# Performance work log

Hardware: AMD Instinct MI355X
Metric: run time of the kernel (lower is better)

Reference implementation:

```python
import jax, jax.numpy as jnp
import numpy as np

D_MODEL = 256
SCALE = jnp.sqrt(jnp.float32(D_MODEL))


def setup_inputs() -> dict:
    key = jax.random.key(0)
    kq, kk, kv = jax.random.split(key, 3)
    B, S, D = 4, 4096, D_MODEL
    Q = jax.random.normal(kq, (B, S, D), dtype=jnp.float32)
    K = jax.random.normal(kk, (B, S, D), dtype=jnp.float32)
    V = jax.random.normal(kv, (B, S, D), dtype=jnp.float32)
    return {"Q": Q, "K": K, "V": V}


def reference(Q, K, V):
    # scores: (B, S, S) = Q @ K^T / sqrt(d_model)
    scores = jnp.einsum('bqd,bkd->bqk', Q, K) / SCALE
    attn = jax.nn.softmax(scores, axis=-1)
    # output: (B, S, D)
    return jnp.einsum('bqk,bkd->bqd', attn, V)
```

## Files before the change

### kernel.cpp

```cpp
#include <hip/hip_runtime.h>
#include <hip/hip_bf16.h>
#include <stdint.h>

#define S_LEN 4096
#define D_DIM 256
#define NBATCH 4
#define NSUP 32

typedef unsigned short u16;
typedef float  f32x4  __attribute__((ext_vector_type(4)));
typedef __bf16 bf16x8 __attribute__((ext_vector_type(8)));
typedef __bf16 bf16x4 __attribute__((ext_vector_type(4)));
typedef short  s16x8  __attribute__((ext_vector_type(8)));
typedef short  s16x4  __attribute__((ext_vector_type(4)));

#define AS1 __attribute__((address_space(1)))
#define AS3 __attribute__((address_space(3)))

__device__ __forceinline__ f32x4 mfma16(bf16x8 a, bf16x8 b, f32x4 c) {
  return __builtin_amdgcn_mfma_f32_16x16x32_bf16(a, b, c, 0, 0, 0);
}

__device__ __forceinline__ s16x4 cvt4(float x, float y, float z, float w) {
  bf16x4 b;
  b[0] = (__bf16)x; b[1] = (__bf16)y; b[2] = (__bf16)z; b[3] = (__bf16)w;
  return __builtin_bit_cast(s16x4, b);
}

__device__ __forceinline__ void gload16(const void* g, void* l) {
  __builtin_amdgcn_global_load_lds((const AS1 unsigned int*)g,
                                   (AS3 unsigned int*)l, 16, 0, 0);
}


__global__ void build_kimg(const float* __restrict__ K, u16* __restrict__ img) {
  const int wg  = blockIdx.x;
  const int tid = threadIdx.x;
  const float* src = K + (size_t)wg * 64 * D_DIM;
  u16*         dst = img + (size_t)wg * 16384;
  #pragma unroll
  for (int i = 0; i < 8; ++i) {
    const int idx = i * 256 + tid;
    const int k = idx >> 5, p = idx & 31;
    const int q = p ^ (k & 7);
    const float* s = src + k * 256 + q * 8;
    float4 f0 = *reinterpret_cast<const float4*>(s);
    float4 f1 = *reinterpret_cast<const float4*>(s + 4);
    s16x8 v = __builtin_shufflevector(cvt4(f0.x, f0.y, f0.z, f0.w),
                                      cvt4(f1.x, f1.y, f1.z, f1.w),
                                      0, 1, 2, 3, 4, 5, 6, 7);
    *reinterpret_cast<s16x8*>(dst + k * 256 + p * 8) = v;
  }
}

__global__ void build_vimg(const float* __restrict__ V, u16* __restrict__ img) {
  __shared__ u16 lds[64 * 264];
  const int wg  = blockIdx.x;
  const int tid = threadIdx.x;
  const float* src = V + (size_t)wg * 64 * D_DIM;
  u16*         dst = img + (size_t)wg * 16384;
  #pragma unroll
  for (int i = 0; i < 8; ++i) {
    const int idx = i * 256 + tid;
    const int k = idx >> 5, q = idx & 31;
    const float* s = src + k * 256 + q * 8;
    float4 f0 = *reinterpret_cast<const float4*>(s);
    float4 f1 = *reinterpret_cast<const float4*>(s + 4);
    s16x8 v = __builtin_shufflevector(cvt4(f0.x, f0.y, f0.z, f0.w),
                                      cvt4(f1.x, f1.y, f1.z, f1.w),
                                      0, 1, 2, 3, 4, 5, 6, 7);
    *reinterpret_cast<s16x8*>(&lds[k * 264 + q * 8]) = v;
  }
  __syncthreads();
  #pragma unroll
  for (int i = 0; i < 8; ++i) {
    const int idx = i * 256 + tid;
    const int d = idx >> 3, c = idx & 7;
    const int cp = c ^ (d & 7);
    s16x8 o;
    #pragma unroll
    for (int j = 0; j < 8; ++j) {
      const int col = 8 * cp + j;
      const int k = (col & 3) + 4 * (col >> 4) + 16 * ((col >> 2) & 3);
      o[j] = (short)lds[k * 264 + d];
    }
    *reinterpret_cast<s16x8*>(dst + d * 64 + c * 8) = o;
  }
}

__device__ __forceinline__
void compute_tile(const char* KsB, const char* vpA, const char* vpB,
                  const bf16x8 (&qf)[8], f32x4 (&acc)[16],
                  float& m_run, float& l_run, int g, int h)
{
  const f32x4 fz = {0.f, 0.f, 0.f, 0.f};

  f32x4 st[4];
  __builtin_amdgcn_s_setprio(1);
  #pragma unroll
  for (int t = 0; t < 4; ++t) {
    f32x4 a = fz;
    const int row = t * 16 + h;
    const int sw  = (row & 7) << 4;
    #pragma unroll
    for (int dc = 0; dc < 8; ++dc) {
      s16x8 kfrag = *reinterpret_cast<const s16x8*>(KsB + row * 512 + ((dc * 64 + g * 16) ^ sw));
      a = mfma16(__builtin_bit_cast(bf16x8, kfrag), qf[dc], a);
    }
    st[t] = a;
  }
  __builtin_amdgcn_s_setprio(0);

  float sv[16];
  #pragma unroll
  for (int t = 0; t < 4; ++t) {
    sv[t * 4 + 0] = st[t][0]; sv[t * 4 + 1] = st[t][1];
    sv[t * 4 + 2] = st[t][2]; sv[t * 4 + 3] = st[t][3];
  }
  float tmax = sv[0];
  #pragma unroll
  for (int i = 1; i < 16; ++i) tmax = fmaxf(tmax, sv[i]);
  tmax = fmaxf(tmax, __shfl_xor(tmax, 16));
  tmax = fmaxf(tmax, __shfl_xor(tmax, 32));

  if (!__all(tmax <= m_run + 8.0f)) {
    const float mnew  = fmaxf(m_run, tmax);
    const float alpha = __expf(m_run - mnew);
    l_run *= alpha;
    const float af0 = __shfl(alpha, g * 4 + 0);
    const float af1 = __shfl(alpha, g * 4 + 1);
    const float af2 = __shfl(alpha, g * 4 + 2);
    const float af3 = __shfl(alpha, g * 4 + 3);
    #pragma unroll
    for (int dt = 0; dt < 16; ++dt) {
      acc[dt][0] *= af0; acc[dt][1] *= af1; acc[dt][2] *= af2; acc[dt][3] *= af3;
    }
    m_run = mnew;
  }

  float psum = 0.f;
  #pragma unroll
  for (int i = 0; i < 16; ++i) { sv[i] = __expf(sv[i] - m_run); psum += sv[i]; }
  psum += __shfl_xor(psum, 16);
  psum += __shfl_xor(psum, 32);
  l_run += psum;

  bf16x8 pa0, pa1;
  #pragma unroll
  for (int j = 0; j < 8; ++j) { pa0[j] = (__bf16)sv[j]; pa1[j] = (__bf16)sv[8 + j]; }

  __builtin_amdgcn_s_setprio(1);
  #pragma unroll
  for (int dt = 0; dt < 16; ++dt) {
    s16x8 v0 = *reinterpret_cast<const s16x8*>(vpA + dt * 2048);
    s16x8 v1 = *reinterpret_cast<const s16x8*>(vpB + dt * 2048);
    acc[dt] = mfma16(pa0, __builtin_bit_cast(bf16x8, v0), acc[dt]);
    acc[dt] = mfma16(pa1, __builtin_bit_cast(bf16x8, v1), acc[dt]);
  }
  __builtin_amdgcn_s_setprio(0);
}

__device__ __forceinline__
void stage_img(const u16* KimgB, const u16* VimgB, int T,
               char* KsB, char* VtB, int w, int lane)
{
  const char* ks = (const char*)(KimgB + (size_t)T * 16384) + lane * 16;
  const char* vs = (const char*)(VimgB + (size_t)T * 16384) + lane * 16;
  #pragma unroll
  for (int i = 0; i < 8; ++i) {
    const int off = (i * 4 + w) * 1024;
    gload16(ks + off, KsB + off);
    gload16(vs + off, VtB + off);
  }
}

template<bool USE_WS>
__global__ __launch_bounds__(512, 1)
void attn_fwd_kernel(const float* __restrict__ Qg, const void* __restrict__ Kp,
                     const void* __restrict__ Vp, float* __restrict__ Og)
{
  __shared__ __align__(16) char smem[131072];

  const int wg   = blockIdx.x;
  const int swz  = (wg & 7) * 32 + (wg >> 3);
  const int b    = swz >> 6;
  const int qt   = swz & 63;
  const int tid  = threadIdx.x;
  const int wave = tid >> 6;
  const int lane = tid & 63;
  const int g    = lane >> 4;
  const int h    = lane & 15;
  const int gid  = tid >> 8;
  const int ltid = tid & 255;
  const int wq   = wave & 3;
  const int w    = wave & 3;

  const int kb  = ltid & 15;
  const int dcq = ltid >> 4;
  const int Xw  = 32 * (kb & 3) + 8 * (kb >> 2);

  char* KsB = smem + gid * 65536;
  char* VtB = KsB + 32768;

  const int qbase = qt * 64 + wq * 16;

  bf16x8 qf[8];
  {
    const float* qrow = Qg + ((size_t)b * S_LEN + qbase + h) * D_DIM;
    #pragma unroll
    for (int dc = 0; dc < 8; ++dc) {
      float4 f0 = *reinterpret_cast<const float4*>(qrow + dc * 32 + g * 8);
      float4 f1 = *reinterpret_cast<const float4*>(qrow + dc * 32 + g * 8 + 4);
      bf16x8 q;
      q[0] = (__bf16)(f0.x * 0.0625f); q[1] = (__bf16)(f0.y * 0.0625f);
      q[2] = (__bf16)(f0.z * 0.0625f); q[3] = (__bf16)(f0.w * 0.0625f);
      q[4] = (__bf16)(f1.x * 0.0625f); q[5] = (__bf16)(f1.y * 0.0625f);
      q[6] = (__bf16)(f1.z * 0.0625f); q[7] = (__bf16)(f1.w * 0.0625f);
      qf[dc] = q;
    }
  }

  f32x4 acc[16];
  const f32x4 fz = {0.f, 0.f, 0.f, 0.f};
  #pragma unroll
  for (int i = 0; i < 16; ++i) acc[i] = fz;
  float m_run = -1e30f;
  float l_run = 0.f;

  const char* vpA = VtB + h * 128 + ((32 * g)      ^ ((h & 7) << 4));
  const char* vpB = VtB + h * 128 + ((32 * g + 16) ^ ((h & 7) << 4));

  if constexpr (USE_WS) {
    const u16* KimgB = (const u16*)Kp + (size_t)b * 64 * 16384;
    const u16* VimgB = (const u16*)Vp + (size_t)b * 64 * 16384;

    if (gid == 0) stage_img(KimgB, VimgB, 0, KsB, VtB, w, lane);
    __syncthreads();

    for (int s = 0; s < NSUP; ++s) {
      if (gid == 0) compute_tile(KsB, vpA, vpB, qf, acc, m_run, l_run, g, h);
      else          stage_img(KimgB, VimgB, 2 * s + 1, KsB, VtB, w, lane);
      __syncthreads();
      if (gid == 0) { if (s < NSUP - 1) stage_img(KimgB, VimgB, 2 * s + 2, KsB, VtB, w, lane); }
      else          compute_tile(KsB, vpA, vpB, qf, acc, m_run, l_run, g, h);
      __syncthreads();
    }

  } else {
    const float* Kf = (const float*)Kp + (size_t)b * S_LEN * D_DIM;
    const float* Vf = (const float*)Vp + (size_t)b * S_LEN * D_DIM;
    for (int s = 0; s < NSUP; ++s) {
      const int kt = 2 * s + gid;
      __syncthreads();
      #pragma unroll
      for (int i = 0; i < 16; ++i) {
        int flat = i * 256 + ltid;
        int kk = flat >> 6;
        int d  = (flat & 63) * 4;
        float4 fk = *reinterpret_cast<const float4*>(Kf + (size_t)(kt * 64 + kk) * D_DIM + d);
        *reinterpret_cast<s16x4*>(KsB + kk * 512 + ((d * 2) ^ ((kk & 7) << 4))) = cvt4(fk.x, fk.y, fk.z, fk.w);
      }
      {
        s16x8 lo[4], hi[4];
        #pragma unroll
        for (int r = 0; r < 4; ++r) {
          const float* src = Vf + (size_t)(kt * 64 + kb * 4 + r) * D_DIM + dcq * 16;
          float4 f0 = *reinterpret_cast<const float4*>(src);
          float4 f1 = *reinterpret_cast<const float4*>(src + 4);
          float4 f2 = *reinterpret_cast<const float4*>(src + 8);
          float4 f3 = *reinterpret_cast<const float4*>(src + 12);
          lo[r] = __builtin_shufflevector(cvt4(f0.x, f0.y, f0.z, f0.w),
                                          cvt4(f1.x, f1.y, f1.z, f1.w), 0, 1, 2, 3, 4, 5, 6, 7);
          hi[r] = __builtin_shufflevector(cvt4(f2.x, f2.y, f2.z, f2.w),
                                          cvt4(f3.x, f3.y, f3.z, f3.w), 0, 1, 2, 3, 4, 5, 6, 7);
        }
        #pragma unroll
        for (int j = 0; j < 8; ++j) {
          s16x4 c0, c1;
          c0[0] = lo[0][j]; c0[1] = lo[1][j]; c0[2] = lo[2][j]; c0[3] = lo[3][j];
          c1[0] = hi[0][j]; c1[1] = hi[1][j]; c1[2] = hi[2][j]; c1[3] = hi[3][j];
          const int d0 = dcq * 16 + j;
          const int d1 = d0 + 8;
          *reinterpret_cast<s16x4*>(VtB + d0 * 128 + (Xw ^ ((d0 & 7) << 4))) = c0;
          *reinterpret_cast<s16x4*>(VtB + d1 * 128 + (Xw ^ ((d1 & 7) << 4))) = c1;
        }
      }
      __syncthreads();
      compute_tile(KsB, vpA, vpB, qf, acc, m_run, l_run, g, h);
    }
  }

  __syncthreads();
  float2* mlM = reinterpret_cast<float2*>(smem + 65536);
  if (gid == 1) {
    const int bw = wave - 4;
    char* base = smem + bw * 16384 + lane * 256;
    #pragma unroll
    for (int dt = 0; dt < 16; ++dt) {
      float4 v; v.x = acc[dt][0]; v.y = acc[dt][1]; v.z = acc[dt][2]; v.w = acc[dt][3];
      *reinterpret_cast<float4*>(base + (dt * 16 ^ ((lane & 7) << 4))) = v;
    }
    if (g == 0) { float2 ml; ml.x = m_run; ml.y = l_run; mlM[bw * 16 + h] = ml; }
  }
  __syncthreads();
  if (gid == 0) {
    const float2 ml = mlM[wave * 16 + h];
    const float mB = ml.x, lB = ml.y;
    const float m  = fmaxf(m_run, mB);
    const float sA = __expf(m_run - m);
    const float sB = __expf(mB - m);
    const float l  = l_run * sA + lB * sB;
    float aA[4], aB[4], inv[4];
    #pragma unroll
    for (int r = 0; r < 4; ++r) {
      aA[r]  = __shfl(sA, g * 4 + r);
      aB[r]  = __shfl(sB, g * 4 + r);
      inv[r] = 1.f / __shfl(l, g * 4 + r);
    }
    const char* base = smem + wave * 16384 + lane * 256;
    float* orow0 = Og + ((size_t)b * S_LEN + qbase) * D_DIM;
    #pragma unroll
    for (int dt = 0; dt < 16; ++dt) {
      float4 ab = *reinterpret_cast<const float4*>(base + (dt * 16 ^ ((lane & 7) << 4)));
      orow0[(size_t)(g * 4 + 0) * D_DIM + h + dt * 16] = (acc[dt][0] * aA[0] + ab.x * aB[0]) * inv[0];
      orow0[(size_t)(g * 4 + 1) * D_DIM + h + dt * 16] = (acc[dt][1] * aA[1] + ab.y * aB[1]) * inv[1];
      orow0[(size_t)(g * 4 + 2) * D_DIM + h + dt * 16] = (acc[dt][2] * aA[2] + ab.z * aB[2]) * inv[2];
      orow0[(size_t)(g * 4 + 3) * D_DIM + h + dt * 16] = (acc[dt][3] * aA[3] + ab.w * aB[3]) * inv[3];
    }
  }
}

extern "C" void kernel_launch(void* const* d_in, const int* in_sizes, int n_in,
                              void* d_out, int out_size, void* d_ws, size_t ws_size,
                              hipStream_t stream)
{
  const float* Q = (const float*)d_in[0];
  const float* K = (const float*)d_in[1];
  const float* V = (const float*)d_in[2];
  float* O = (float*)d_out;

  const size_t nelem = (size_t)NBATCH * S_LEN * D_DIM;
  const size_t need  = 2 * nelem * sizeof(u16);

  if (ws_size >= need) {
    u16* Kimg = (u16*)d_ws;
    u16* Vimg = Kimg + nelem;
    build_kimg<<<256, 256, 0, stream>>>(K, Kimg);
    build_vimg<<<256, 256, 0, stream>>>(V, Vimg);
    attn_fwd_kernel<true><<<256, 512, 0, stream>>>(Q, (const void*)Kimg, (const void*)Vimg, O);
  } else {
    attn_fwd_kernel<false><<<256, 512, 0, stream>>>(Q, (const void*)K, (const void*)V, O);
  }
}
```

Before: 126.1 us.

## Shrink Q and KV tiles to 32 and run two 256-thread blocks per CU

Halves the query tile per workgroup (32 rows, 4 waves) and the KV block (32 keys), doubling the grid to 512 blocks with two resident per CU. V image layout and swizzle are reworked for 32-key blocks, and each compute step uses one PV MFMA per dt. The goal is better occupancy and CU fill across 256 CUs. The cost is twice the K/V reads per query row and more per-tile softmax overhead.

Measured after the change: 164.6 us. 1.31x slower.

```diff
diff --git a/kernel.cpp b/kernel.cpp
--- a/kernel.cpp
+++ b/kernel.cpp
@@ -5,7 +5,8 @@
 #define S_LEN 4096
 #define D_DIM 256
 #define NBATCH 4
-#define NSUP 32
+#define KVBLK 32
+#define NSUP 64
 
 typedef unsigned short u16;
 typedef float  f32x4  __attribute__((ext_vector_type(4)));
@@ -33,13 +34,13 @@
 }
 
 
-__global__ void build_kimg(const float* __restrict__ K, u16* __restrict__ img) {
+__global__ void build_kimg32(const float* __restrict__ K, u16* __restrict__ img) {
   const int wg  = blockIdx.x;
   const int tid = threadIdx.x;
-  const float* src = K + (size_t)wg * 64 * D_DIM;
-  u16*         dst = img + (size_t)wg * 16384;
-  #pragma unroll
-  for (int i = 0; i < 8; ++i) {
+  const float* src = K + (size_t)wg * KVBLK * D_DIM;
+  u16*         dst = img + (size_t)wg * 8192;
+  #pragma unroll
+  for (int i = 0; i < 4; ++i) {
     const int idx = i * 256 + tid;
     const int k = idx >> 5, p = idx & 31;
     const int q = p ^ (k & 7);
@@ -53,14 +54,14 @@
   }
 }
 
-__global__ void build_vimg(const float* __restrict__ V, u16* __restrict__ img) {
-  __shared__ u16 lds[64 * 264];
+__global__ void build_vimg32(const float* __restrict__ V, u16* __restrict__ img) {
+  __shared__ u16 lds[KVBLK * 264];
   const int wg  = blockIdx.x;
   const int tid = threadIdx.x;
-  const float* src = V + (size_t)wg * 64 * D_DIM;
-  u16*         dst = img + (size_t)wg * 16384;
-  #pragma unroll
-  for (int i = 0; i < 8; ++i) {
+  const float* src = V + (size_t)wg * KVBLK * D_DIM;
+  u16*         dst = img + (size_t)wg * 8192;
+  #pragma unroll
+  for (int i = 0; i < 4; ++i) {
     const int idx = i * 256 + tid;
     const int k = idx >> 5, q = idx & 31;
     const float* s = src + k * 256 + q * 8;
@@ -72,54 +73,52 @@
     *reinterpret_cast<s16x8*>(&lds[k * 264 + q * 8]) = v;
   }
   __syncthreads();
-  #pragma unroll
-  for (int i = 0; i < 8; ++i) {
-    const int idx = i * 256 + tid;
-    const int d = idx >> 3, c = idx & 7;
-    const int cp = c ^ (d & 7);
+  const int d = tid;
+  const int s = ((d >> 4) ^ d) & 3;
+  #pragma unroll
+  for (int c = 0; c < 4; ++c) {
+    const int gp = c ^ s;
     s16x8 o;
     #pragma unroll
-    for (int j = 0; j < 8; ++j) {
-      const int col = 8 * cp + j;
-      const int k = (col & 3) + 4 * (col >> 4) + 16 * ((col >> 2) & 3);
-      o[j] = (short)lds[k * 264 + d];
-    }
-    *reinterpret_cast<s16x8*>(dst + d * 64 + c * 8) = o;
+    for (int ii = 0; ii < 8; ++ii) {
+      const int k = 16 * (ii >> 2) + 4 * gp + (ii & 3);
+      o[ii] = (short)lds[k * 264 + d];
+    }
+    *reinterpret_cast<s16x8*>(dst + d * 32 + c * 8) = o;
   }
 }
 
 __device__ __forceinline__
-void compute_tile(const char* KsB, const char* vpA, const char* vpB,
-                  const bf16x8 (&qf)[8], f32x4 (&acc)[16],
-                  float& m_run, float& l_run, int g, int h)
+void compute_tile32(const char* KsB, const char* VtB,
+                    const bf16x8 (&qf)[8], f32x4 (&acc)[16],
+                    float& m_run, float& l_run, int g, int h)
 {
   const f32x4 fz = {0.f, 0.f, 0.f, 0.f};
 
-  f32x4 st[4];
+  f32x4 st[2];
+  st[0] = fz; st[1] = fz;
   __builtin_amdgcn_s_setprio(1);
   #pragma unroll
-  for (int t = 0; t < 4; ++t) {
-    f32x4 a = fz;
+  for (int t = 0; t < 2; ++t) {
     const int row = t * 16 + h;
     const int sw  = (row & 7) << 4;
     #pragma unroll
     for (int dc = 0; dc < 8; ++dc) {
-      s16x8 kfrag = *reinterpret_cast<const s16x8*>(KsB + row * 512 + ((dc * 64 + g * 16) ^ sw));
-      a = mfma16(__builtin_bit_cast(bf16x8, kfrag), qf[dc], a);
-    }
-    st[t] = a;
+      s16x8 kf = *reinterpret_cast<const s16x8*>(KsB + row * 512 + ((dc * 64 + g * 16) ^ sw));
+      st[t] = mfma16(__builtin_bit_cast(bf16x8, kf), qf[dc], st[t]);
+    }
   }
   __builtin_amdgcn_s_setprio(0);
 
-  float sv[16];
-  #pragma unroll
-  for (int t = 0; t < 4; ++t) {
+  float sv[8];
+  #pragma unroll
+  for (int t = 0; t < 2; ++t) {
     sv[t * 4 + 0] = st[t][0]; sv[t * 4 + 1] = st[t][1];
     sv[t * 4 + 2] = st[t][2]; sv[t * 4 + 3] = st[t][3];
   }
   float tmax = sv[0];
   #pragma unroll
-  for (int i = 1; i < 16; ++i) tmax = fmaxf(tmax, sv[i]);
+  for (int i = 1; i < 8; ++i) tmax = fmaxf(tmax, sv[i]);
   tmax = fmaxf(tmax, __shfl_xor(tmax, 16));
   tmax = fmaxf(tmax, __shfl_xor(tmax, 32));
 
@@ -127,82 +126,80 @@
     const float mnew  = fmaxf(m_run, tmax);
     const float alpha = __expf(m_run - mnew);
     l_run *= alpha;
-    const float af0 = __shfl(alpha, g * 4 + 0);
-    const float af1 = __shfl(alpha, g * 4 + 1);
-    const float af2 = __shfl(alpha, g * 4 + 2);
-    const float af3 = __shfl(alpha, g * 4 + 3);
+    float af[4];
+    #pragma unroll
+    for (int r = 0; r < 4; ++r) af[r] = __shfl(alpha, g * 4 + r);
     #pragma unroll
     for (int dt = 0; dt < 16; ++dt) {
-      acc[dt][0] *= af0; acc[dt][1] *= af1; acc[dt][2] *= af2; acc[dt][3] *= af3;
+      acc[dt][0] *= af[0]; acc[dt][1] *= af[1];
+      acc[dt][2] *= af[2]; acc[dt][3] *= af[3];
     }
     m_run = mnew;
   }
 
   float psum = 0.f;
   #pragma unroll
-  for (int i = 0; i < 16; ++i) { sv[i] = __expf(sv[i] - m_run); psum += sv[i]; }
+  for (int i = 0; i < 8; ++i) { sv[i] = __expf(sv[i] - m_run); psum += sv[i]; }
   psum += __shfl_xor(psum, 16);
   psum += __shfl_xor(psum, 32);
   l_run += psum;
 
-  bf16x8 pa0, pa1;
-  #pragma unroll
-  for (int j = 0; j < 8; ++j) { pa0[j] = (__bf16)sv[j]; pa1[j] = (__bf16)sv[8 + j]; }
+  bf16x8 pa;
+  #pragma unroll
+  for (int j = 0; j < 8; ++j) pa[j] = (__bf16)sv[j];
 
   __builtin_amdgcn_s_setprio(1);
   #pragma unroll
   for (int dt = 0; dt < 16; ++dt) {
-    s16x8 v0 = *reinterpret_cast<const s16x8*>(vpA + dt * 2048);
-    s16x8 v1 = *reinterpret_cast<const s16x8*>(vpB + dt * 2048);
-    acc[dt] = mfma16(pa0, __builtin_bit_cast(bf16x8, v0), acc[dt]);
-    acc[dt] = mfma16(pa1, __builtin_bit_cast(bf16x8, v1), acc[dt]);
+    const int d = dt * 16 + h;
+    s16x8 vf = *reinterpret_cast<const s16x8*>(VtB + d * 64 + ((16 * g) ^ (((dt ^ h) & 3) << 4)));
+    acc[dt] = mfma16(pa, __builtin_bit_cast(bf16x8, vf), acc[dt]);
   }
   __builtin_amdgcn_s_setprio(0);
 }
 
 __device__ __forceinline__
-void stage_img(const u16* KimgB, const u16* VimgB, int T,
-               char* KsB, char* VtB, int w, int lane)
+void stage_img32(const u16* KimgB, const u16* VimgB, int T,
+                 char* KsB, char* VtB, int gl)
 {
-  const char* ks = (const char*)(KimgB + (size_t)T * 16384) + lane * 16;
-  const char* vs = (const char*)(VimgB + (size_t)T * 16384) + lane * 16;
+  const char* ks = (const char*)(KimgB + (size_t)T * 8192) + gl * 16;
+  const char* vs = (const char*)(VimgB + (size_t)T * 8192) + gl * 16;
   #pragma unroll
   for (int i = 0; i < 8; ++i) {
-    const int off = (i * 4 + w) * 1024;
-    gload16(ks + off, KsB + off);
-    gload16(vs + off, VtB + off);
+    gload16(ks + i * 2048, KsB + gl * 16 + i * 2048);
+    gload16(vs + i * 2048, VtB + gl * 16 + i * 2048);
   }
 }
 
 template<bool USE_WS>
-__global__ __launch_bounds__(512, 1)
+__global__ __launch_bounds__(256, 2)
 void attn_fwd_kernel(const float* __restrict__ Qg, const void* __restrict__ Kp,
                      const void* __restrict__ Vp, float* __restrict__ Og)
 {
-  __shared__ __align__(16) char smem[131072];
+  __shared__ __align__(16) char smem[66048];
 
   const int wg   = blockIdx.x;
-  const int swz  = (wg & 7) * 32 + (wg >> 3);
-  const int b    = swz >> 6;
-  const int qt   = swz & 63;
+  const int swz  = (wg & 7) * 64 + (wg >> 3);
+  const int b    = swz >> 7;
+  const int qt   = swz & 127;
   const int tid  = threadIdx.x;
   const int wave = tid >> 6;
   const int lane = tid & 63;
   const int g    = lane >> 4;
   const int h    = lane & 15;
-  const int gid  = tid >> 8;
-  const int ltid = tid & 255;
-  const int wq   = wave & 3;
-  const int w    = wave & 3;
-
-  const int kb  = ltid & 15;
-  const int dcq = ltid >> 4;
-  const int Xw  = 32 * (kb & 3) + 8 * (kb >> 2);
-
-  char* KsB = smem + gid * 65536;
-  char* VtB = KsB + 32768;
-
-  const int qbase = qt * 64 + wq * 16;
+  const int gid  = wave >> 1;
+  const int wq   = wave & 1;
+  const int ltid = tid & 127;
+
+  const int kb  = ltid & 7;
+  const int dcq = ltid >> 3;
+  const int Xw  = 16 * (kb & 3) + 8 * (kb >> 2);
+
+  char* KsB = smem + gid * 32768;
+  char* VtB = KsB + 16384;
+  float2* mlM = reinterpret_cast<float2*>(smem + 65536);
+
+  const int qbase = qt * 32 + wq * 16;
 
   bf16x8 qf[8];
   {
@@ -227,44 +224,43 @@
   float m_run = -1e30f;
   float l_run = 0.f;
 
-  const char* vpA = VtB + h * 128 + ((32 * g)      ^ ((h & 7) << 4));
-  const char* vpB = VtB + h * 128 + ((32 * g + 16) ^ ((h & 7) << 4));
-
   if constexpr (USE_WS) {
-    const u16* KimgB = (const u16*)Kp + (size_t)b * 64 * 16384;
-    const u16* VimgB = (const u16*)Vp + (size_t)b * 64 * 16384;
-
-    if (gid == 0) stage_img(KimgB, VimgB, 0, KsB, VtB, w, lane);
+    const u16* KimgB = (const u16*)Kp + (size_t)b * 128 * 8192;
+    const u16* VimgB = (const u16*)Vp + (size_t)b * 128 * 8192;
+
+    if (gid == 0) stage_img32(KimgB, VimgB, 0, KsB, VtB, ltid);
     __syncthreads();
 
     for (int s = 0; s < NSUP; ++s) {
-      if (gid == 0) compute_tile(KsB, vpA, vpB, qf, acc, m_run, l_run, g, h);
-      else          stage_img(KimgB, VimgB, 2 * s + 1, KsB, VtB, w, lane);
+      if (gid == 0) compute_tile32(KsB, VtB, qf, acc, m_run, l_run, g, h);
+      else          stage_img32(KimgB, VimgB, 2 * s + 1, KsB, VtB, ltid);
       __syncthreads();
-      if (gid == 0) { if (s < NSUP - 1) stage_img(KimgB, VimgB, 2 * s + 2, KsB, VtB, w, lane); }
-      else          compute_tile(KsB, vpA, vpB, qf, acc, m_run, l_run, g, h);
+      if (gid == 0) { if (s < NSUP - 1) stage_img32(KimgB, VimgB, 2 * s + 2, KsB, VtB, ltid); }
+      else          compute_tile32(KsB, VtB, qf, acc, m_run, l_run, g, h);
       __syncthreads();
     }
 
   } else {
     const float* Kf = (const float*)Kp + (size_t)b * S_LEN * D_DIM;
     const float* Vf = (const float*)Vp + (size_t)b * S_LEN * D_DIM;
+    const int rk = ltid >> 2, ck = ltid & 3;
     for (int s = 0; s < NSUP; ++s) {
-      const int kt = 2 * s + gid;
+      const int tile = 2 * s + gid;
       __syncthreads();
       #pragma unroll
-      for (int i = 0; i < 16; ++i) {
-        int flat = i * 256 + ltid;
-        int kk = flat >> 6;
-        int d  = (flat & 63) * 4;
-        float4 fk = *reinterpret_cast<const float4*>(Kf + (size_t)(kt * 64 + kk) * D_DIM + d);
-        *reinterpret_cast<s16x4*>(KsB + kk * 512 + ((d * 2) ^ ((kk & 7) << 4))) = cvt4(fk.x, fk.y, fk.z, fk.w);
+      for (int i = 0; i < 8; ++i) {
+        const float* src = Kf + (size_t)(tile * KVBLK + rk) * D_DIM + ck * 64 + i * 8;
+        float4 f0 = *reinterpret_cast<const float4*>(src);
+        float4 f1 = *reinterpret_cast<const float4*>(src + 4);
+        char* dst = KsB + rk * 512 + ((ck * 128 + i * 16) ^ ((rk & 7) << 4));
+        *reinterpret_cast<s16x4*>(dst)     = cvt4(f0.x, f0.y, f0.z, f0.w);
+        *reinterpret_cast<s16x4*>(dst + 8) = cvt4(f1.x, f1.y, f1.z, f1.w);
       }
       {
         s16x8 lo[4], hi[4];
         #pragma unroll
         for (int r = 0; r < 4; ++r) {
-          const float* src = Vf + (size_t)(kt * 64 + kb * 4 + r) * D_DIM + dcq * 16;
+          const float* src = Vf + (size_t)(tile * KVBLK + kb * 4 + r) * D_DIM + dcq * 16;
           float4 f0 = *reinterpret_cast<const float4*>(src);
           float4 f1 = *reinterpret_cast<const float4*>(src + 4);
           float4 f2 = *reinterpret_cast<const float4*>(src + 8);
@@ -281,19 +277,18 @@
           c1[0] = hi[0][j]; c1[1] = hi[1][j]; c1[2] = hi[2][j]; c1[3] = hi[3][j];
           const int d0 = dcq * 16 + j;
           const int d1 = d0 + 8;
-          *reinterpret_cast<s16x4*>(VtB + d0 * 128 + (Xw ^ ((d0 & 7) << 4))) = c0;
-          *reinterpret_cast<s16x4*>(VtB + d1 * 128 + (Xw ^ ((d1 & 7) << 4))) = c1;
+          *reinterpret_cast<s16x4*>(VtB + d0 * 64 + (Xw ^ ((((d0 >> 4) ^ d0) & 3) << 4))) = c0;
+          *reinterpret_cast<s16x4*>(VtB + d1 * 64 + (Xw ^ ((((d1 >> 4) ^ d1) & 3) << 4))) = c1;
         }
       }
       __syncthreads();
-      compute_tile(KsB, vpA, vpB, qf, acc, m_run, l_run, g, h);
+      compute_tile32(KsB, VtB, qf, acc, m_run, l_run, g, h);
     }
   }
 
   __syncthreads();
-  float2* mlM = reinterpret_cast<float2*>(smem + 65536);
   if (gid == 1) {
-    const int bw = wave - 4;
+    const int bw = wave - 2;
     char* base = smem + bw * 16384 + lane * 256;
     #pragma unroll
     for (int dt = 0; dt < 16; ++dt) {
@@ -345,10 +340,10 @@
   if (ws_size >= need) {
     u16* Kimg = (u16*)d_ws;
     u16* Vimg = Kimg + nelem;
-    build_kimg<<<256, 256, 0, stream>>>(K, Kimg);
-    build_vimg<<<256, 256, 0, stream>>>(V, Vimg);
-    attn_fwd_kernel<true><<<256, 512, 0, stream>>>(Q, (const void*)Kimg, (const void*)Vimg, O);
+    build_kimg32<<<512, 256, 0, stream>>>(K, Kimg);
+    build_vimg32<<<512, 256, 0, stream>>>(V, Vimg);
+    attn_fwd_kernel<true><<<512, 256, 0, stream>>>(Q, (const void*)Kimg, (const void*)Vimg, O);
   } else {
-    attn_fwd_kernel<false><<<256, 512, 0, stream>>>(Q, (const void*)K, (const void*)V, O);
-  }
-}
+    attn_fwd_kernel<false><<<512, 256, 0, stream>>>(Q, (const void*)K, (const void*)V, O);
+  }
+}
```
